# Kernel tuning notes

Measured on AMD Instinct MI355X. Metric: run time of the kernel, lower is better.

Reference implementation:

```python
import jax, jax.numpy as jnp
import numpy as np

N, D, E = 100000, 128, 1600000
BN_SCALE = 1.0 / np.sqrt(1.0 + 1e-3)  # Keras BN at inference with init stats: x/sqrt(var+eps)


def bn(x):
    return x * jnp.asarray(BN_SCALE, x.dtype)


def l2norm(x):
    s = jnp.sum(x * x, axis=1, keepdims=True)
    return x * jax.lax.rsqrt(jnp.maximum(s, 1e-12))


def spmm(rows, cols, vals, h, n):
    # (sparse NxN) @ (dense NxD) via gather + segment_sum
    return jax.ops.segment_sum(vals[:, None] * h[cols], rows, num_segments=n)


def setup_inputs() -> dict:
    key = jax.random.key(0)
    ks = jax.random.split(key, 12)
    g = 1.0 / np.sqrt(D)  # glorot-ish scale
    return {
        "x": jax.random.normal(ks[0], (N, D), jnp.float32),
        "a1_rows": jax.random.randint(ks[1], (E,), 0, N, jnp.int32),
        "a1_cols": jax.random.randint(ks[2], (E,), 0, N, jnp.int32),
        "a1_vals": jax.random.uniform(ks[3], (E,), jnp.float32),
        "a2_rows": jax.random.randint(ks[4], (E,), 0, N, jnp.int32),
        "a2_cols": jax.random.randint(ks[5], (E,), 0, N, jnp.int32),
        "a2_vals": jnp.ones((E,), jnp.float32),
        "w_gcn1": jax.random.normal(ks[6], (D, D), jnp.float32) * g,
        "b_gcn1": jnp.zeros((D,), jnp.float32),
        "w_att": jax.random.normal(ks[7], (D, D), jnp.float32) * g,
        "m1": jax.random.normal(ks[8], (D, D), jnp.float32) * g,
        "m2": jax.random.normal(ks[9], (D, D), jnp.float32) * g,
        "w_hw": jax.random.normal(ks[10], (D, D), jnp.float32) * g,
        "w_gcn2": jax.random.normal(ks[11], (D, D), jnp.float32) * g,
        "b_gcn2": jnp.zeros((D,), jnp.float32),
    }


def gcn_layer(x, rows, cols, vals, w, b, n):
    xb = bn(x)
    return jnp.tanh(spmm(rows, cols, vals, xb @ w, n) + b)


def atten_layer(x, rows, cols, vals, w, m1, m2, n):
    xb = bn(x)
    mapped = xb @ w  # [N, D]
    s1 = jnp.tanh(jnp.sum((xb @ m1) * xb, axis=1))  # [N]
    s2 = jnp.tanh(jnp.sum((xb @ m2) * xb, axis=1))  # [N]
    # per-edge score: A*s1[row] + A^T-broadcast s2[col], then leaky_relu (tf alpha=0.2)
    e = jax.nn.leaky_relu(vals * s1[rows] + vals * s2[cols], negative_slope=0.2)
    # sparse row-wise softmax
    mx = jax.ops.segment_max(e, rows, num_segments=n)
    ex = jnp.exp(e - mx[rows])
    denom = jax.ops.segment_sum(ex, rows, num_segments=n)
    a = ex / denom[rows]
    return spmm(rows, cols, a / jnp.maximum(vals, 1e-30) * vals * 0 + a, mapped, n) if False else jax.ops.segment_sum(a[:, None] * mapped[cols], rows, num_segments=n)


def highway_layer(y_att, y_gcn, w):
    i1 = bn(y_att)
    i2 = bn(y_gcn)
    gate = jax.nn.relu(jnp.tanh(i1 @ w))
    return jnp.tanh(i2 * (1.0 - gate) + i1 * gate)


def reference(x, a1_rows, a1_cols, a1_vals, a2_rows, a2_cols, a2_vals,
              w_gcn1, b_gcn1, w_att, m1, m2, w_hw, w_gcn2, b_gcn2):
    n = x.shape[0]
    y1 = gcn_layer(x, a1_rows, a1_cols, a1_vals, w_gcn1, b_gcn1, n)
    y2 = atten_layer(x, a2_rows, a2_cols, a2_vals, w_att, m1, m2, n)
    y3 = highway_layer(y2, y1, w_hw)
    y4 = gcn_layer(y3, a1_rows, a1_cols, a1_vals, w_gcn2, b_gcn2, n)
    y = jnp.concatenate([l2norm(y3), l2norm(y4), l2norm(x)], axis=1)
    return l2norm(y)
```

## Files before the change

kernel.cpp:

```cpp
#include <hip/hip_runtime.h>
#include <hip/hip_fp16.h>
#include <math.h>
#include <stdint.h>

#define DD 128
#define BSH 9

typedef _Float16 f16;
typedef _Float16 f16x8 __attribute__((ext_vector_type(8)));
typedef float f32x4 __attribute__((ext_vector_type(4)));

__global__ __launch_bounds__(256) void k_ph(
    const float* __restrict__ w0, const float* __restrict__ w1, const float* __restrict__ w2,
    const float* __restrict__ w3, const float* __restrict__ w4, const float* __restrict__ w5,
    f16* __restrict__ wh,
    const int* __restrict__ r1, const int* __restrict__ r2, int* __restrict__ hist,
    int E, int tile, int nt){
  __shared__ __align__(16) unsigned char smem[128*136*2];
  int t = threadIdx.x;
  if((int)blockIdx.x < 6){
    auto tw = (f16 (*)[136])smem;
    int b = blockIdx.x;
    const float* W = (b==0)?w0:(b==1)?w1:(b==2)?w2:(b==3)?w3:(b==4)?w4:w5;
    for(int j=0;j<16;++j){
      int f = j*256+t; int k = f>>5, c4 = f&31;
      float4 v = *(const float4*)(W + (size_t)k*DD + c4*4);
      tw[c4*4+0][k]=(f16)v.x; tw[c4*4+1][k]=(f16)v.y; tw[c4*4+2][k]=(f16)v.z; tw[c4*4+3][k]=(f16)v.w;
    }
    __syncthreads();
    f16* dst = wh + (size_t)b*16384;
    for(int j=0;j<8;++j){
      int f = j*256+t; int c = f>>4, seg = f&15;
      *(int4*)&dst[(size_t)c*DD + seg*8] = *(int4*)&tw[c][seg*8];
    }
  } else {
    int* h1 = (int*)smem; int* h2 = h1+256;
    h1[t]=0; h2[t]=0; __syncthreads();
    int hb = blockIdx.x - 6;
    int e0 = hb*tile, e1 = min(e0+tile, E);
    for(int e=e0+t; e<e1; e+=256){
      atomicAdd(&h1[r1[e]>>BSH], 1);
      atomicAdd(&h2[r2[e]>>BSH], 1);
    }
    __syncthreads();
    hist[(size_t)hb*256 + t] = h1[t];
    hist[(size_t)nt*256 + (size_t)hb*256 + t] = h2[t];
  }
}

__global__ void k_colscan(int* __restrict__ hist, int* __restrict__ colsum, int nt){
  __shared__ int sh[256];
  int g = blockIdx.x>>8, b = blockIdx.x&255;
  int t = threadIdx.x;
  int* H = hist + (size_t)g*nt*256;
  int v = (t<nt)? H[(size_t)t*256+b] : 0;
  sh[t]=v; __syncthreads();
  for(int off=1; off<256; off<<=1){
    int add = (t>=off)? sh[t-off] : 0;
    __syncthreads(); sh[t]+=add; __syncthreads();
  }
  if(t<nt) H[(size_t)t*256+b] = sh[t]-v;
  if(t==255) colsum[g*256+b] = sh[255];
}

__global__ void k_basescan(const int* __restrict__ colsum, int* __restrict__ base){
  __shared__ int sh[512];
  int t = threadIdx.x;
  int g = t>>8, st = t&255;
  int v = colsum[t];
  sh[t]=v; __syncthreads();
  for(int off=1; off<256; off<<=1){
    int add = (st>=off)? sh[t-off] : 0;
    __syncthreads(); sh[t]+=add; __syncthreads();
  }
  base[g*257+st] = sh[t]-v;
  if(st==255) base[g*257+256] = sh[t];
}

__global__ __launch_bounds__(256) void k_px(
    const int* __restrict__ r1, const int* __restrict__ c1, const float* __restrict__ v1,
    const int* __restrict__ r2, const int* __restrict__ c2,
    const int* __restrict__ hist, const int* __restrict__ base,
    int2* __restrict__ st1, int* __restrict__ st2, int E, int tile, int nt,
    const float* __restrict__ x, const f16* __restrict__ wh,
    f16* __restrict__ h1h, f16* __restrict__ mapped,
    float* __restrict__ s1, float* __restrict__ s2,
    float bn, float sscale, int n){
  __shared__ __align__(16) unsigned char smem[52224];
  int t = threadIdx.x;
  if((int)blockIdx.x < nt){
    int* l1 = (int*)smem; int* l2 = l1+256;
    l1[t]=0; l2[t]=0; __syncthreads();
    int bx = blockIdx.x;
    int e0 = bx*tile, e1e = min(e0+tile, E);
    const int* off1 = hist + (size_t)bx*256;
    const int* off2 = hist + (size_t)nt*256 + (size_t)bx*256;
    for(int e=e0+t; e<e1e; e+=256){
      {
        int r = r1[e]; int b = r>>BSH;
        int rank = atomicAdd(&l1[b], 1);
        int dst = base[b] + off1[b] + rank;
        st1[dst] = make_int2(((r - (b<<BSH))<<17) | c1[e], __float_as_int(v1[e]));
      }
      {
        int r = r2[e]; int b = r>>BSH;
        int rank = atomicAdd(&l2[b], 1);
        int dst = base[257+b] + off2[b] + rank;
        st2[dst] = ((r - (b<<BSH))<<17) | c2[e];
      }
    }
  } else {
    auto at = (f16 (*)[136])smem;
    auto wt = (f16 (*)[136])(smem + 64*136*2);
    int r0 = (blockIdx.x - nt)*64;
    int l = t&63, w = t>>6, li = l&15, g = l>>4;
    for(int p=0;p<4;++p){
      int row = p*16 + (t>>4), seg = t&15;
      union{ f16 h[8]; int4 v; } u;
      u.v = make_int4(0,0,0,0);
      if(r0+row < n){
        const float* src = x + (size_t)(r0+row)*DD + seg*8;
        float4 a = *(const float4*)src, b = *(const float4*)(src+4);
        u.h[0]=(f16)a.x; u.h[1]=(f16)a.y; u.h[2]=(f16)a.z; u.h[3]=(f16)a.w;
        u.h[4]=(f16)b.x; u.h[5]=(f16)b.y; u.h[6]=(f16)b.z; u.h[7]=(f16)b.w;
      }
      *(int4*)&at[row][seg*8] = u.v;
    }
    for(int p=0;p<4;++p){
      __syncthreads();
      const f16* Wp = wh + (size_t)p*16384;
      for(int j=0;j<8;++j){
        int f = j*256+t; int c = f>>4, seg = f&15;
        *(int4*)&wt[c][seg*8] = *(const int4*)(Wp + (size_t)c*DD + seg*8);
      }
      __syncthreads();
      f32x4 acc[8];
      #pragma unroll
      for(int ct=0;ct<8;++ct) acc[ct] = (f32x4){0.f,0.f,0.f,0.f};
      #pragma unroll
      for(int ks=0;ks<4;++ks){
        f16x8 a = *(const f16x8*)&at[w*16+li][ks*32+g*8];
        #pragma unroll
        for(int ct=0;ct<8;++ct){
          f16x8 b = *(const f16x8*)&wt[ct*16+li][ks*32+g*8];
          acc[ct] = __builtin_amdgcn_mfma_f32_16x16x32_f16(a, b, acc[ct], 0,0,0);
        }
      }
      if(p<2){
        f16* out = p ? mapped : h1h;
        __syncthreads();
        #pragma unroll
        for(int ct=0;ct<8;++ct)
          #pragma unroll
          for(int reg=0;reg<4;++reg)
            wt[w*16+g*4+reg][ct*16+li] = (f16)(acc[ct][reg]*bn);
        __syncthreads();
        for(int j=0;j<4;++j){
          int f = j*256+t; int row = f>>4, seg = f&15;
          if(r0+row < n) *(int4*)&out[(size_t)(r0+row)*DD + seg*8] = *(int4*)&wt[row][seg*8];
        }
      } else {
        float* sd = (p==2) ? s1 : s2;
        #pragma unroll
        for(int reg=0;reg<4;++reg){
          float pd = 0.f;
          #pragma unroll
          for(int ct=0;ct<8;++ct)
            pd += acc[ct][reg]*(float)at[w*16+g*4+reg][ct*16+li];
          pd += __shfl_xor(pd,1,64); pd += __shfl_xor(pd,2,64);
          pd += __shfl_xor(pd,4,64); pd += __shfl_xor(pd,8,64);
          if(li==0){
            int grow = r0 + w*16 + g*4 + reg;
            if(grow < n) sd[grow] = tanhf(sscale*pd);
          }
        }
      }
    }
  }
}

__global__ void k_csr_bucket(const int2* __restrict__ st1, const int* __restrict__ st2,
                             const int* __restrict__ base,
                             int2* __restrict__ e1, int* __restrict__ e2,
                             int* __restrict__ rs, int N, int nbk){
  __shared__ int cnt[512];
  __shared__ int cur[512];
  __shared__ int sc[256];
  int g = blockIdx.x / nbk;
  int b = blockIdx.x % nbk;
  int t = threadIdx.x;
  cnt[t]=0; cnt[256+t]=0;
  __syncthreads();
  int ebeg = base[g*257+b], eend = base[g*257+b+1];
  if(g==0){
    for(int i=ebeg+t; i<eend; i+=256) atomicAdd(&cnt[st1[i].x>>17], 1);
  } else {
    for(int i=ebeg+t; i<eend; i+=256) atomicAdd(&cnt[st2[i]>>17], 1);
  }
  __syncthreads();
  int a0 = cnt[2*t], a1 = cnt[2*t+1];
  int s = a0+a1;
  sc[t]=s; __syncthreads();
  for(int off=1; off<256; off<<=1){
    int add = (t>=off)? sc[t-off] : 0;
    __syncthreads(); sc[t]+=add; __syncthreads();
  }
  int ex = sc[t]-s;
  cur[2*t] = ex; cur[2*t+1] = ex + a0;
  __syncthreads();
  int r0 = b<<BSH;
  int* rsg = rs + (size_t)g*(N+1);
  for(int i=t; i<512; i+=256){
    int r = r0+i;
    if(r<N) rsg[r] = ebeg + cur[i];
  }
  if(b==nbk-1 && t==0) rsg[N] = base[g*257+256];
  __syncthreads();
  if(g==0){
    for(int i=ebeg+t; i<eend; i+=256){
      int2 w = st1[i];
      int lr = w.x>>17;
      int p = ebeg + atomicAdd(&cur[lr], 1);
      e1[p] = make_int2(w.x & 0x1FFFF, w.y);
    }
  } else {
    for(int i=ebeg+t; i<eend; i+=256){
      int w = st2[i];
      int lr = w>>17;
      int p = ebeg + atomicAdd(&cur[lr], 1);
      e2[p] = w & 0x1FFFF;
    }
  }
}

__global__ __launch_bounds__(256) void k_hw2(
    const f16* __restrict__ y2h, const f16* __restrict__ y1h,
    const f16* __restrict__ wh, f16* __restrict__ y3h, f16* __restrict__ h3h,
    float bn, int n){
  __shared__ __align__(16) f16 at[64][136];
  __shared__ __align__(16) f16 wt[128][136];
  int t = threadIdx.x;
  int r0 = blockIdx.x*64;
  int l = t&63, w = t>>6, li = l&15, g = l>>4;
  for(int p=0;p<4;++p){
    int row = p*16 + (t>>4), seg = t&15;
    int4 v = make_int4(0,0,0,0);
    if(r0+row < n) v = *(const int4*)(y2h + (size_t)(r0+row)*DD + seg*8);
    *(int4*)&at[row][seg*8] = v;
  }
  __syncthreads();
  for(int j=0;j<8;++j){
    int f = j*256+t; int c = f>>4, seg = f&15;
    *(int4*)&wt[c][seg*8] = *(const int4*)(wh + (size_t)4*16384 + (size_t)c*DD + seg*8);
  }
  __syncthreads();
  f32x4 acc[8];
  #pragma unroll
  for(int ct=0;ct<8;++ct) acc[ct] = (f32x4){0.f,0.f,0.f,0.f};
  #pragma unroll
  for(int ks=0;ks<4;++ks){
    f16x8 a = *(const f16x8*)&at[w*16+li][ks*32+g*8];
    #pragma unroll
    for(int ct=0;ct<8;++ct){
      f16x8 b = *(const f16x8*)&wt[ct*16+li][ks*32+g*8];
      acc[ct] = __builtin_amdgcn_mfma_f32_16x16x32_f16(a, b, acc[ct], 0,0,0);
    }
  }
  float res[8][4];
  #pragma unroll
  for(int ct=0;ct<8;++ct)
    #pragma unroll
    for(int reg=0;reg<4;++reg){
      int lrow = w*16+g*4+reg, col = ct*16+li;
      int grow = r0+lrow;
      float gt = tanhf(bn*acc[ct][reg]); gt = fmaxf(gt, 0.f);
      float y1v = (grow<n)? (float)y1h[(size_t)grow*DD+col] : 0.f;
      float y2v = (float)at[lrow][col];
      res[ct][reg] = tanhf(bn*(y1v*(1.f-gt) + y2v*gt));
    }
  #pragma unroll
  for(int ct=0;ct<8;++ct)
    #pragma unroll
    for(int reg=0;reg<4;++reg)
      at[w*16+g*4+reg][ct*16+li] = (f16)res[ct][reg];
  __syncthreads();
  for(int j=0;j<4;++j){
    int f = j*256+t; int row = f>>4, seg = f&15;
    if(r0+row < n) *(int4*)&y3h[(size_t)(r0+row)*DD + seg*8] = *(int4*)&at[row][seg*8];
  }
  __syncthreads();
  for(int j=0;j<8;++j){
    int f = j*256+t; int c = f>>4, seg = f&15;
    *(int4*)&wt[c][seg*8] = *(const int4*)(wh + (size_t)5*16384 + (size_t)c*DD + seg*8);
  }
  __syncthreads();
  #pragma unroll
  for(int ct=0;ct<8;++ct) acc[ct] = (f32x4){0.f,0.f,0.f,0.f};
  #pragma unroll
  for(int ks=0;ks<4;++ks){
    f16x8 a = *(const f16x8*)&at[w*16+li][ks*32+g*8];
    #pragma unroll
    for(int ct=0;ct<8;++ct){
      f16x8 b = *(const f16x8*)&wt[ct*16+li][ks*32+g*8];
      acc[ct] = __builtin_amdgcn_mfma_f32_16x16x32_f16(a, b, acc[ct], 0,0,0);
    }
  }
  __syncthreads();
  #pragma unroll
  for(int ct=0;ct<8;++ct)
    #pragma unroll
    for(int reg=0;reg<4;++reg)
      wt[w*16+g*4+reg][ct*16+li] = (f16)(acc[ct][reg]*bn);
  __syncthreads();
  for(int j=0;j<4;++j){
    int f = j*256+t; int row = f>>4, seg = f&15;
    if(r0+row < n) *(int4*)&h3h[(size_t)(r0+row)*DD + seg*8] = *(int4*)&wt[row][seg*8];
  }
}

__device__ __forceinline__ void spmm_row16(const int* __restrict__ rs, const int2* __restrict__ e1,
                                           const __half* __restrict__ h, const float* __restrict__ bias,
                                           __half* __restrict__ out, int row, int l ){
  int beg = rs[row], end = rs[row+1];
  float a[8] = {0.f,0.f,0.f,0.f,0.f,0.f,0.f,0.f};
  for(int k=beg; k<end; k+=8){
    int2 cv[8];
    union{ uint4 v; __half2 h2[4]; } hh[8];
    #pragma unroll
    for(int j=0;j<8;++j){ int kk = min(k+j, end-1); cv[j] = e1[kk]; }
    #pragma unroll
    for(int j=0;j<8;++j) hh[j].v = ((const uint4*)(h + (size_t)cv[j].x*DD))[l];
    #pragma unroll
    for(int j=0;j<8;++j){
      float v = (k+j<end)? __int_as_float(cv[j].y) : 0.f;
      #pragma unroll
      for(int q=0;q<4;++q){
        float2 f = __half22float2(hh[j].h2[q]);
        a[2*q]   += v*f.x;
        a[2*q+1] += v*f.y;
      }
    }
  }
  float4 b0 = ((const float4*)bias)[2*l], b1 = ((const float4*)bias)[2*l+1];
  union{ uint4 v; __half2 h2[4]; } o;
  o.h2[0] = __floats2half2_rn(tanhf(a[0]+b0.x), tanhf(a[1]+b0.y));
  o.h2[1] = __floats2half2_rn(tanhf(a[2]+b0.z), tanhf(a[3]+b0.w));
  o.h2[2] = __floats2half2_rn(tanhf(a[4]+b1.x), tanhf(a[5]+b1.y));
  o.h2[3] = __floats2half2_rn(tanhf(a[6]+b1.z), tanhf(a[7]+b1.w));
  ((uint4*)(out + (size_t)row*DD))[l] = o.v;
}

__device__ __forceinline__ void attn_row16(const int* __restrict__ rs, const int* __restrict__ e2,
                                           const float* __restrict__ s1, const float* __restrict__ s2,
                                           const __half* __restrict__ mapped, __half* __restrict__ out,
                                           int row, int l){
  int beg = rs[row], end = rs[row+1];
  float s1r = s1[row];
  float a[8] = {0.f,0.f,0.f,0.f,0.f,0.f,0.f,0.f};
  float den = 0.f;
  for(int k=beg; k<end; k+=8){
    int cs[8]; float sv[8];
    union{ uint4 v; __half2 h2[4]; } mh[8];
    #pragma unroll
    for(int j=0;j<8;++j){ int kk = min(k+j, end-1); cs[j] = e2[kk]; }
    #pragma unroll
    for(int j=0;j<8;++j) sv[j] = s2[cs[j]];
    #pragma unroll
    for(int j=0;j<8;++j) mh[j].v = ((const uint4*)(mapped + (size_t)cs[j]*DD))[l];
    #pragma unroll
    for(int j=0;j<8;++j){
      float e = s1r + sv[j]; e = (e>=0.f)? e : 0.2f*e;
      float ex = (k+j<end)? __expf(e) : 0.f;
      den += ex;
      #pragma unroll
      for(int q=0;q<4;++q){
        float2 f = __half22float2(mh[j].h2[q]);
        a[2*q]   += ex*f.x;
        a[2*q+1] += ex*f.y;
      }
    }
  }
  float inv = (end > beg) ? 1.0f/den : 0.0f;
  union{ uint4 v; __half2 h2[4]; } o;
  o.h2[0] = __floats2half2_rn(a[0]*inv, a[1]*inv);
  o.h2[1] = __floats2half2_rn(a[2]*inv, a[3]*inv);
  o.h2[2] = __floats2half2_rn(a[4]*inv, a[5]*inv);
  o.h2[3] = __floats2half2_rn(a[6]*inv, a[7]*inv);
  ((uint4*)(out + (size_t)row*DD))[l] = o.v;
}

__global__ void k_agg1(const int* __restrict__ rs, const int2* __restrict__ e1,
                       const __half* __restrict__ h1h, const float* __restrict__ b1, __half* __restrict__ y1h,
                       const int* __restrict__ e2, const float* __restrict__ s1, const float* __restrict__ s2,
                       const __half* __restrict__ mapped, __half* __restrict__ y2h,
                       int n, int gT){
  int l = threadIdx.x & 15;
  if((int)blockIdx.x < gT){
    int row = blockIdx.x*16 + (threadIdx.x>>4);
    if(row>=n) return;
    spmm_row16(rs, e1, h1h, b1, y1h, row, l);
  } else {
    int row = (blockIdx.x-gT)*16 + (threadIdx.x>>4);
    if(row>=n) return;
    attn_row16(rs+(n+1), e2, s1, s2, mapped, y2h, row, l);
  }
}

__global__ void k_spmm2(const int* __restrict__ rs, const int2* __restrict__ e1,
                        const __half* __restrict__ h, const float* __restrict__ bias,
                        __half* __restrict__ out, int n){
  int row = blockIdx.x*16 + (threadIdx.x>>4);
  if(row>=n) return;
  spmm_row16(rs, e1, h, bias, out, row, threadIdx.x & 15);
}

__global__ void k_final(const __half* __restrict__ y3, const __half* __restrict__ y4,
                        const float* __restrict__ x, float* __restrict__ out, int n){
  int row = blockIdx.x*4 + (threadIdx.x>>6);
  if(row>=n) return;
  int lane = threadIdx.x & 63;
  float2 a = __half22float2(((const __half2*)(y3 + (size_t)row*DD))[lane]);
  float2 b = __half22float2(((const __half2*)(y4 + (size_t)row*DD))[lane]);
  float2 c = ((const float2*)(x  + (size_t)row*DD))[lane];
  float sa = a.x*a.x + a.y*a.y;
  float sb = b.x*b.x + b.y*b.y;
  float sc = c.x*c.x + c.y*c.y;
  #pragma unroll
  for(int off=32; off; off>>=1){
    sa += __shfl_xor(sa, off, 64);
    sb += __shfl_xor(sb, off, 64);
    sc += __shfl_xor(sc, off, 64);
  }
  float ia = rsqrtf(fmaxf(sa, 1e-12f));
  float ib = rsqrtf(fmaxf(sb, 1e-12f));
  float ic = rsqrtf(fmaxf(sc, 1e-12f));
  float tot = sa*ia*ia + sb*ib*ib + sc*ic*ic;
  float f = rsqrtf(fmaxf(tot, 1e-12f));
  float fa = ia*f, fb = ib*f, fc = ic*f;
  float2* o = (float2*)(out + (size_t)row*(3*DD));
  o[lane]     = make_float2(a.x*fa, a.y*fa);
  o[64+lane]  = make_float2(b.x*fb, b.y*fb);
  o[128+lane] = make_float2(c.x*fc, c.y*fc);
}

extern "C" void kernel_launch(void* const* d_in, const int* in_sizes, int n_in,
                              void* d_out, int out_size, void* d_ws, size_t ws_size,
                              hipStream_t stream){
  const float* x   = (const float*)d_in[0];
  const int*   a1r = (const int*)d_in[1];
  const int*   a1c = (const int*)d_in[2];
  const float* a1v = (const float*)d_in[3];
  const int*   a2r = (const int*)d_in[4];
  const int*   a2c = (const int*)d_in[5];
  const float* w1  = (const float*)d_in[7];
  const float* b1  = (const float*)d_in[8];
  const float* watt= (const float*)d_in[9];
  const float* m1  = (const float*)d_in[10];
  const float* m2  = (const float*)d_in[11];
  const float* whw = (const float*)d_in[12];
  const float* w2  = (const float*)d_in[13];
  const float* b2  = (const float*)d_in[14];

  const int N = in_sizes[0]/DD;
  const int E = in_sizes[1];
  const float BN = (float)(1.0/sqrt(1.0+1e-3));
  const size_t NB = (size_t)N*DD;

  int tile = 8192, nt = (E+tile-1)/tile;
  while(nt > 256){ tile <<= 1; nt = (E+tile-1)/tile; }
  const int nbk = (N + (1<<BSH) - 1) >> BSH;

  f16* Bh = (f16*)d_ws;
  f16* Ch = Bh + NB;
  f16* Dh = Ch + NB;
  f16* Eh = Dh + NB;
  f16* wh = Eh + NB;
  float* s1 = (float*)(wh + 6*16384);
  float* s2 = s1 + N;
  int*  rs  = (int*)(s2 + N);
  uintptr_t pa = ((uintptr_t)(rs + 2*(N+1)) + 15) & ~(uintptr_t)15;
  int2* e1  = (int2*)pa;
  int*  e2  = (int*)(e1 + E);
  uintptr_t pb = ((uintptr_t)(e2 + E) + 15) & ~(uintptr_t)15;
  int2* st1 = (int2*)pb;
  int*  st2 = (int*)(st1 + E);
  int*  hist = st2 + E;
  int*  colsum = hist + (size_t)2*nt*256;
  int*  base = colsum + 512;

  const int gR = (N+3)/4;
  const int gT = (N+15)/16;
  const int gM = (N+63)/64;
  float* out = (float*)d_out;

  k_ph<<<6+nt,256,0,stream>>>(w1, watt, m1, m2, whw, w2, wh, a1r, a2r, hist, E, tile, nt);

  k_colscan<<<512,256,0,stream>>>(hist, colsum, nt);
  k_basescan<<<1,512,0,stream>>>(colsum, base);

  k_px<<<nt+gM,256,0,stream>>>(a1r,a1c,a1v, a2r,a2c, hist, base, st1, st2, E, tile, nt,
                               x, wh, Bh, Ch, s1, s2, BN, BN*BN, N);

  k_csr_bucket<<<2*nbk,256,0,stream>>>(st1, st2, base, e1, e2, rs, N, nbk);

  k_agg1<<<2*gT,256,0,stream>>>(rs, e1, (const __half*)Bh, b1, (__half*)Dh,
                                e2, s1, s2, (const __half*)Ch, (__half*)Eh, N, gT);

  k_hw2<<<gM,256,0,stream>>>(Eh, Dh, wh, Ch, Bh, BN, N);

  k_spmm2<<<gT,256,0,stream>>>(rs, e1, (const __half*)Bh, b2, (__half*)Dh, N);

  k_final<<<gR,256,0,stream>>>((const __half*)Ch, (const __half*)Dh, x, out, N);
}
```

Measured before the change: 425.1 us.

## Accumulate SpMM in packed fp16 and fuse second GCN with final normalization

Switches the SpMM and attention aggregation accumulators from fp32 scalar FMAs to packed fp16x2 multiply-adds, halving ALU work in the gather loops. It also fuses the second GCN SpMM with the final L2-normalization/concat kernel, so y4 is never written to and re-read from global memory and one launch is removed. The fp16 accumulation over about 16 edges per row risks precision loss and overflow relative to the fp32 reference.

```diff
diff --git a/kernel.cpp b/kernel.cpp
--- a/kernel.cpp
+++ b/kernel.cpp
@@ -7,6 +7,7 @@
 #define BSH 9
 
 typedef _Float16 f16;
+typedef _Float16 f16x2 __attribute__((ext_vector_type(2)));
 typedef _Float16 f16x8 __attribute__((ext_vector_type(8)));
 typedef float f32x4 __attribute__((ext_vector_type(4)));
 
@@ -318,14 +319,15 @@
   }
 }
 
-__device__ __forceinline__ void spmm_row16(const int* __restrict__ rs, const int2* __restrict__ e1,
-                                           const __half* __restrict__ h, const float* __restrict__ bias,
-                                           __half* __restrict__ out, int row, int l ){
+__device__ __forceinline__ void spmm_row16_h(const int* __restrict__ rs, const int2* __restrict__ e1,
+                                             const __half* __restrict__ h, int row, int l,
+                                             f16x2 acc2[4]){
   int beg = rs[row], end = rs[row+1];
-  float a[8] = {0.f,0.f,0.f,0.f,0.f,0.f,0.f,0.f};
+  #pragma unroll
+  for(int q=0;q<4;++q) acc2[q] = (f16x2){(f16)0.f,(f16)0.f};
   for(int k=beg; k<end; k+=8){
     int2 cv[8];
-    union{ uint4 v; __half2 h2[4]; } hh[8];
+    union{ uint4 v; f16x2 h2[4]; } hh[8];
     #pragma unroll
     for(int j=0;j<8;++j){ int kk = min(k+j, end-1); cv[j] = e1[kk]; }
     #pragma unroll
@@ -333,21 +335,12 @@
     #pragma unroll
     for(int j=0;j<8;++j){
       float v = (k+j<end)? __int_as_float(cv[j].y) : 0.f;
+      f16 vh = (f16)v;
+      f16x2 vv = {vh, vh};
       #pragma unroll
-      for(int q=0;q<4;++q){
-        float2 f = __half22float2(hh[j].h2[q]);
-        a[2*q]   += v*f.x;
-        a[2*q+1] += v*f.y;
-      }
-    }
-  }
-  float4 b0 = ((const float4*)bias)[2*l], b1 = ((const float4*)bias)[2*l+1];
-  union{ uint4 v; __half2 h2[4]; } o;
-  o.h2[0] = __floats2half2_rn(tanhf(a[0]+b0.x), tanhf(a[1]+b0.y));
-  o.h2[1] = __floats2half2_rn(tanhf(a[2]+b0.z), tanhf(a[3]+b0.w));
-  o.h2[2] = __floats2half2_rn(tanhf(a[4]+b1.x), tanhf(a[5]+b1.y));
-  o.h2[3] = __floats2half2_rn(tanhf(a[6]+b1.z), tanhf(a[7]+b1.w));
-  ((uint4*)(out + (size_t)row*DD))[l] = o.v;
+      for(int q=0;q<4;++q) acc2[q] += hh[j].h2[q]*vv;
+    }
+  }
 }
 
 __device__ __forceinline__ void attn_row16(const int* __restrict__ rs, const int* __restrict__ e2,
@@ -356,11 +349,13 @@
                                            int row, int l){
   int beg = rs[row], end = rs[row+1];
   float s1r = s1[row];
-  float a[8] = {0.f,0.f,0.f,0.f,0.f,0.f,0.f,0.f};
+  f16x2 a2[4];
+  #pragma unroll
+  for(int q=0;q<4;++q) a2[q] = (f16x2){(f16)0.f,(f16)0.f};
   float den = 0.f;
   for(int k=beg; k<end; k+=8){
     int cs[8]; float sv[8];
-    union{ uint4 v; __half2 h2[4]; } mh[8];
+    union{ uint4 v; f16x2 h2[4]; } mh[8];
     #pragma unroll
     for(int j=0;j<8;++j){ int kk = min(k+j, end-1); cs[j] = e2[kk]; }
     #pragma unroll
@@ -372,20 +367,17 @@
       float e = s1r + sv[j]; e = (e>=0.f)? e : 0.2f*e;
       float ex = (k+j<end)? __expf(e) : 0.f;
       den += ex;
+      f16 xh = (f16)ex;
+      f16x2 xx = {xh, xh};
       #pragma unroll
-      for(int q=0;q<4;++q){
-        float2 f = __half22float2(mh[j].h2[q]);
-        a[2*q]   += ex*f.x;
-        a[2*q+1] += ex*f.y;
-      }
+      for(int q=0;q<4;++q) a2[q] += mh[j].h2[q]*xx;
     }
   }
   float inv = (end > beg) ? 1.0f/den : 0.0f;
   union{ uint4 v; __half2 h2[4]; } o;
-  o.h2[0] = __floats2half2_rn(a[0]*inv, a[1]*inv);
-  o.h2[1] = __floats2half2_rn(a[2]*inv, a[3]*inv);
-  o.h2[2] = __floats2half2_rn(a[4]*inv, a[5]*inv);
-  o.h2[3] = __floats2half2_rn(a[6]*inv, a[7]*inv);
+  #pragma unroll
+  for(int q=0;q<4;++q)
+    o.h2[q] = __floats2half2_rn((float)a2[q].x*inv, (float)a2[q].y*inv);
   ((uint4*)(out + (size_t)row*DD))[l] = o.v;
 }
 
@@ -398,7 +390,15 @@
   if((int)blockIdx.x < gT){
     int row = blockIdx.x*16 + (threadIdx.x>>4);
     if(row>=n) return;
-    spmm_row16(rs, e1, h1h, b1, y1h, row, l);
+    f16x2 acc2[4];
+    spmm_row16_h(rs, e1, h1h, row, l, acc2);
+    float4 b0 = ((const float4*)b1)[2*l], bb1 = ((const float4*)b1)[2*l+1];
+    union{ uint4 v; __half2 h2[4]; } o;
+    o.h2[0] = __floats2half2_rn(tanhf((float)acc2[0].x+b0.x), tanhf((float)acc2[0].y+b0.y));
+    o.h2[1] = __floats2half2_rn(tanhf((float)acc2[1].x+b0.z), tanhf((float)acc2[1].y+b0.w));
+    o.h2[2] = __floats2half2_rn(tanhf((float)acc2[2].x+bb1.x), tanhf((float)acc2[2].y+bb1.y));
+    o.h2[3] = __floats2half2_rn(tanhf((float)acc2[3].x+bb1.z), tanhf((float)acc2[3].y+bb1.w));
+    ((uint4*)(y1h + (size_t)row*DD))[l] = o.v;
   } else {
     int row = (blockIdx.x-gT)*16 + (threadIdx.x>>4);
     if(row>=n) return;
@@ -406,27 +406,37 @@
   }
 }
 
-__global__ void k_spmm2(const int* __restrict__ rs, const int2* __restrict__ e1,
-                        const __half* __restrict__ h, const float* __restrict__ bias,
-                        __half* __restrict__ out, int n){
+__global__ void k_spmm_final(const int* __restrict__ rs, const int2* __restrict__ e1,
+                             const __half* __restrict__ h, const float* __restrict__ bias,
+                             const __half* __restrict__ y3, const float* __restrict__ x,
+                             float* __restrict__ out, int n){
   int row = blockIdx.x*16 + (threadIdx.x>>4);
   if(row>=n) return;
-  spmm_row16(rs, e1, h, bias, out, row, threadIdx.x & 15);
-}
-
-__global__ void k_final(const __half* __restrict__ y3, const __half* __restrict__ y4,
-                        const float* __restrict__ x, float* __restrict__ out, int n){
-  int row = blockIdx.x*4 + (threadIdx.x>>6);
-  if(row>=n) return;
-  int lane = threadIdx.x & 63;
-  float2 a = __half22float2(((const __half2*)(y3 + (size_t)row*DD))[lane]);
-  float2 b = __half22float2(((const __half2*)(y4 + (size_t)row*DD))[lane]);
-  float2 c = ((const float2*)(x  + (size_t)row*DD))[lane];
-  float sa = a.x*a.x + a.y*a.y;
-  float sb = b.x*b.x + b.y*b.y;
-  float sc = c.x*c.x + c.y*c.y;
-  #pragma unroll
-  for(int off=32; off; off>>=1){
+  int l = threadIdx.x & 15;
+  f16x2 acc2[4];
+  spmm_row16_h(rs, e1, h, row, l, acc2);
+  float4 b0 = ((const float4*)bias)[2*l], b1 = ((const float4*)bias)[2*l+1];
+  float y4v[8];
+  y4v[0]=tanhf((float)acc2[0].x+b0.x); y4v[1]=tanhf((float)acc2[0].y+b0.y);
+  y4v[2]=tanhf((float)acc2[1].x+b0.z); y4v[3]=tanhf((float)acc2[1].y+b0.w);
+  y4v[4]=tanhf((float)acc2[2].x+b1.x); y4v[5]=tanhf((float)acc2[2].y+b1.y);
+  y4v[6]=tanhf((float)acc2[3].x+b1.z); y4v[7]=tanhf((float)acc2[3].y+b1.w);
+  union{ uint4 v; __half2 h2[4]; } y3u;
+  y3u.v = ((const uint4*)(y3 + (size_t)row*DD))[l];
+  float y3v[8];
+  #pragma unroll
+  for(int q=0;q<4;++q){
+    float2 f = __half22float2(y3u.h2[q]);
+    y3v[2*q] = f.x; y3v[2*q+1] = f.y;
+  }
+  const float* xp = x + (size_t)row*DD + l*8;
+  float4 xa = *(const float4*)xp, xb = *(const float4*)(xp+4);
+  float xv[8] = {xa.x,xa.y,xa.z,xa.w,xb.x,xb.y,xb.z,xb.w};
+  float sa=0.f, sb=0.f, sc=0.f;
+  #pragma unroll
+  for(int q=0;q<8;++q){ sa += y3v[q]*y3v[q]; sb += y4v[q]*y4v[q]; sc += xv[q]*xv[q]; }
+  #pragma unroll
+  for(int off=1; off<16; off<<=1){
     sa += __shfl_xor(sa, off, 64);
     sb += __shfl_xor(sb, off, 64);
     sc += __shfl_xor(sc, off, 64);
@@ -437,10 +447,13 @@
   float tot = sa*ia*ia + sb*ib*ib + sc*ic*ic;
   float f = rsqrtf(fmaxf(tot, 1e-12f));
   float fa = ia*f, fb = ib*f, fc = ic*f;
-  float2* o = (float2*)(out + (size_t)row*(3*DD));
-  o[lane]     = make_float2(a.x*fa, a.y*fa);
-  o[64+lane]  = make_float2(b.x*fb, b.y*fb);
-  o[128+lane] = make_float2(c.x*fc, c.y*fc);
+  float* o = out + (size_t)row*(3*DD);
+  *(float4*)(o + l*8)     = make_float4(y3v[0]*fa, y3v[1]*fa, y3v[2]*fa, y3v[3]*fa);
+  *(float4*)(o + l*8 + 4) = make_float4(y3v[4]*fa, y3v[5]*fa, y3v[6]*fa, y3v[7]*fa);
+  *(float4*)(o + DD + l*8)     = make_float4(y4v[0]*fb, y4v[1]*fb, y4v[2]*fb, y4v[3]*fb);
+  *(float4*)(o + DD + l*8 + 4) = make_float4(y4v[4]*fb, y4v[5]*fb, y4v[6]*fb, y4v[7]*fb);
+  *(float4*)(o + 2*DD + l*8)     = make_float4(xv[0]*fc, xv[1]*fc, xv[2]*fc, xv[3]*fc);
+  *(float4*)(o + 2*DD + l*8 + 4) = make_float4(xv[4]*fc, xv[5]*fc, xv[6]*fc, xv[7]*fc);
 }
 
 extern "C" void kernel_launch(void* const* d_in, const int* in_sizes, int n_in,
@@ -488,7 +501,6 @@
   int*  colsum = hist + (size_t)2*nt*256;
   int*  base = colsum + 512;
 
-  const int gR = (N+3)/4;
   const int gT = (N+15)/16;
   const int gM = (N+63)/64;
   float* out = (float*)d_out;
@@ -508,7 +520,6 @@
 
   k_hw2<<<gM,256,0,stream>>>(Eh, Dh, wh, Ch, Bh, BN, N);
 
-  k_spmm2<<<gT,256,0,stream>>>(rs, e1, (const __half*)Bh, b2, (__half*)Dh, N);
-
-  k_final<<<gR,256,0,stream>>>((const __half*)Ch, (const __half*)Dh, x, out, N);
-}
+  k_spmm_final<<<gT,256,0,stream>>>(rs, e1, (const __half*)Bh, b2,
+                                    (const __half*)Ch, x, out, N);
+}
```

Result: faster. 406.9 us (-4.3%).
